# Optimization experiments

Measured on AMD Instinct MI355X. Metric: run time of the kernel, lower is better.

## Reference

```python
import jax, jax.numpy as jnp
import numpy as np

NUM_CLUSTERS = 64  # label vocabulary size (labels in [0, NUM_CLUSTERS))


def setup_inputs() -> dict:
    key = jax.random.key(0)
    kf, kl = jax.random.split(key)
    features = jax.random.normal(kf, (8192, 128), dtype=jnp.float32)
    labels = jax.random.randint(kl, (8192,), 0, NUM_CLUSTERS, dtype=jnp.int64)
    return {"features": features, "labels": labels}


def _pairwise_dist(x):
    # Euclidean cdist with a grad-safe sqrt (zero entries -> zero, no NaN grads).
    sq = jnp.sum(x * x, axis=-1)                      # [N]
    d2 = sq[:, None] + sq[None, :] - 2.0 * (x @ x.T)  # [N, N]
    d2 = jnp.maximum(d2, 0.0)
    pos = d2 > 0
    return jnp.sqrt(jnp.where(pos, d2, 1.0)) * pos.astype(x.dtype)


def reference(features, labels):
    N = features.shape[0]
    C = NUM_CLUSTERS
    dtype = features.dtype

    onehot = jax.nn.one_hot(labels, C, dtype=dtype)   # [N, C]
    counts = jnp.sum(onehot, axis=0)                  # [C]

    dists = _pairwise_dist(features)                  # [N, N]
    # Per-sample sum of distances to each cluster: segment-sum over columns.
    S = dists @ onehot                                # [N, C]

    own_count = counts[labels]                        # [N]
    idx = jnp.arange(N)
    # mean intra-cluster distance a_i (exclude self: divide by n-1)
    a = S[idx, labels] / jnp.maximum(own_count - 1.0, 1.0)

    # mean distance to every other cluster; mask own cluster and empty clusters
    mean_inter = S / jnp.maximum(counts, 1.0)[None, :]          # [N, C]
    invalid = (onehot > 0) | (counts[None, :] == 0)
    big = jnp.asarray(jnp.finfo(dtype).max, dtype)
    b = jnp.min(jnp.where(invalid, big, mean_inter), axis=1)    # [N]

    score = (b - a) / jnp.maximum(b, a)
    # singleton clusters get score 0 (matches torch branch num_elements <= 1)
    score = jnp.where(own_count > 1, score, jnp.zeros((), dtype))
    return jnp.mean(score)
```

## Files before the change

### kernel.cpp

```cpp
#include <hip/hip_runtime.h>
#include <hip/hip_fp16.h>
#include <float.h>

#define NC 64
#define FD 128
#define LSTR 136

typedef _Float16 f16x8 __attribute__((ext_vector_type(8)));
typedef float f32x4 __attribute__((ext_vector_type(4)));

__global__ void prep_kernel(const float* __restrict__ feat,
                            const int* __restrict__ labels,
                            float* __restrict__ sq,
                            unsigned short* __restrict__ Xh,
                            unsigned short* __restrict__ Mt,
                            float* __restrict__ S,
                            float* __restrict__ out, int out_size,
                            int* __restrict__ counts, int N) {
  __shared__ int hist[NC];
  int t = threadIdx.x;
  if (t < NC) hist[t] = 0;
  __syncthreads();
  int row = blockIdx.x * 32 + (t >> 3);
  int o = t & 7;
  if (row < N) {
    const float* rp = feat + (size_t)row * FD;
    float s = 0.f;
#pragma unroll
    for (int j = 0; j < 4; ++j) {
      int c4 = o + 8 * j;
      float4 v = *(const float4*)(rp + c4 * 4);
      ushort4 h;
      h.x = __half_as_ushort(__float2half(v.x));
      h.y = __half_as_ushort(__float2half(v.y));
      h.z = __half_as_ushort(__float2half(v.z));
      h.w = __half_as_ushort(__float2half(v.w));
      *(ushort4*)&Xh[(size_t)row * FD + c4 * 4] = h;
      s = fmaf(v.x, v.x, s); s = fmaf(v.y, v.y, s);
      s = fmaf(v.z, v.z, s); s = fmaf(v.w, v.w, s);
    }
    s += __shfl_xor(s, 1); s += __shfl_xor(s, 2); s += __shfl_xor(s, 4);
    if (o == 0) { sq[row] = s; atomicAdd(&hist[labels[row]], 1); }
  }
  if ((blockIdx.x + 1) * 32 <= N) {
    float4 z = {0.f, 0.f, 0.f, 0.f};
    size_t base = (size_t)blockIdx.x * 32 * NC + t * 8;
    *(float4*)&S[base] = z;
    *(float4*)&S[base + 4] = z;
  }
  if (blockIdx.x == 0 && t < out_size) out[t] = 0.f;
  {
    int chunksPerN = N >> 3;
    int total = NC * chunksPerN;
    for (int id = blockIdx.x * 256 + t; id < total; id += gridDim.x * 256) {
      int n = id / chunksPerN;
      int c0 = (id - n * chunksPerN) * 8;
      ushort4 lo, hi;
      lo.x = (labels[c0 + 0] == n) ? 0x3C00 : 0;
      lo.y = (labels[c0 + 1] == n) ? 0x3C00 : 0;
      lo.z = (labels[c0 + 2] == n) ? 0x3C00 : 0;
      lo.w = (labels[c0 + 3] == n) ? 0x3C00 : 0;
      hi.x = (labels[c0 + 4] == n) ? 0x3C00 : 0;
      hi.y = (labels[c0 + 5] == n) ? 0x3C00 : 0;
      hi.z = (labels[c0 + 6] == n) ? 0x3C00 : 0;
      hi.w = (labels[c0 + 7] == n) ? 0x3C00 : 0;
      *(ushort4*)&Mt[(size_t)n * N + c0] = lo;
      *(ushort4*)&Mt[(size_t)n * N + c0 + 4] = hi;
    }
  }
  __syncthreads();
  if (t < NC) atomicAdd(&counts[t], hist[t]);
}

__global__ __launch_bounds__(256, 2)
void mfma_tile_kernel(const unsigned short* __restrict__ Xh,
                      const float* __restrict__ sq,
                      const unsigned short* __restrict__ Mt,
                      float* __restrict__ S,
                      int N, int colsPerSplit) {
  __shared__ __align__(16) unsigned short Ah[128 * LSTR];
  __shared__ __align__(16) unsigned short Bh[128 * LSTR];

  const int t = threadIdx.x;
  const int R = blockIdx.x * 128;
  const int cBeg = blockIdx.y * colsPerSplit;
  const int wave = t >> 6, lane = t & 63;
  const int mm = lane & 15, quad = lane >> 4;
  const int wr = wave >> 1, wc = wave & 1;

#pragma unroll
  for (int it = 0; it < 8; ++it) {
    int c = t + it * 256;
    int r = c >> 4, k0 = (c & 15) * 8;
    *(uint4*)&Ah[r * LSTR + k0] = *(const uint4*)&Xh[(size_t)(R + r) * FD + k0];
  }
  float sqi_r[4];
#pragma unroll
  for (int ib = 0; ib < 4; ++ib)
    sqi_r[ib] = sq[R + wr * 64 + ib * 16 + mm];

  f32x4 sacc[2][4];
#pragma unroll
  for (int rt = 0; rt < 2; ++rt)
#pragma unroll
    for (int lt = 0; lt < 4; ++lt) sacc[rt][lt] = (f32x4)0.f;

  const int numTiles = colsPerSplit / 128;
  for (int ct = 0; ct < numTiles; ++ct) {
    const int C0 = cBeg + ct * 128;
    __syncthreads();
#pragma unroll
    for (int it = 0; it < 8; ++it) {
      int c = t + it * 256;
      int r = c >> 4, k0 = (c & 15) * 8;
      *(uint4*)&Bh[r * LSTR + k0] = *(const uint4*)&Xh[(size_t)(C0 + r) * FD + k0];
    }
    float sjr[4][4];
#pragma unroll
    for (int jb = 0; jb < 4; ++jb)
#pragma unroll
      for (int r = 0; r < 4; ++r)
        sjr[jb][r] = sq[C0 + wc * 64 + jb * 16 + quad * 4 + r];
    __syncthreads();

    f32x4 dacc[4][4];
#pragma unroll
    for (int ib = 0; ib < 4; ++ib)
#pragma unroll
      for (int jb = 0; jb < 4; ++jb) dacc[ib][jb] = (f32x4)0.f;

#pragma unroll
    for (int ks = 0; ks < 4; ++ks) {
      const int ko = ks * 32 + quad * 8;
      f16x8 af[4], bf[4];
#pragma unroll
      for (int ib = 0; ib < 4; ++ib)
        af[ib] = *(const f16x8*)&Ah[(wr * 64 + ib * 16 + mm) * LSTR + ko];
#pragma unroll
      for (int jb = 0; jb < 4; ++jb)
        bf[jb] = *(const f16x8*)&Bh[(wc * 64 + jb * 16 + mm) * LSTR + ko];
#pragma unroll
      for (int ib = 0; ib < 4; ++ib)
#pragma unroll
        for (int jb = 0; jb < 4; ++jb)
          dacc[ib][jb] = __builtin_amdgcn_mfma_f32_16x16x32_f16(bf[jb], af[ib], dacc[ib][jb], 0, 0, 0);
    }
    __syncthreads();

    const bool hasDiag = (R == C0);
#pragma unroll
    for (int ib = 0; ib < 4; ++ib) {
      const int rowLocal = wr * 64 + ib * 16 + mm;
      const float si = sqi_r[ib];
#pragma unroll
      for (int jb = 0; jb < 4; ++jb) {
        const int colBase = wc * 64 + jb * 16 + quad * 4;
        float d[4];
#pragma unroll
        for (int r = 0; r < 4; ++r) {
          float d2 = fmaf(-2.f, dacc[ib][jb][r], si + sjr[jb][r]);
          d[r] = __builtin_amdgcn_sqrtf(fmaxf(d2, 0.f));
        }
        if (hasDiag) {
#pragma unroll
          for (int r = 0; r < 4; ++r)
            if (rowLocal == colBase + r) d[r] = 0.f;
        }
        uint2 pk;
        pk.x = __builtin_bit_cast(unsigned, __builtin_amdgcn_cvt_pkrtz(d[0], d[1]));
        pk.y = __builtin_bit_cast(unsigned, __builtin_amdgcn_cvt_pkrtz(d[2], d[3]));
        *(uint2*)&Bh[rowLocal * LSTR + colBase] = pk;
      }
    }
    __syncthreads();

#pragma unroll
    for (int ks = 0; ks < 4; ++ks) {
      const int ko = ks * 32 + quad * 8;
      f16x8 da0 = *(const f16x8*)&Bh[(wave * 32 + mm) * LSTR + ko];
      f16x8 da1 = *(const f16x8*)&Bh[(wave * 32 + 16 + mm) * LSTR + ko];
#pragma unroll
      for (int lt = 0; lt < 4; ++lt) {
        f16x8 mb = *(const f16x8*)&Mt[(size_t)(lt * 16 + mm) * N + C0 + ks * 32 + quad * 8];
        sacc[0][lt] = __builtin_amdgcn_mfma_f32_16x16x32_f16(da0, mb, sacc[0][lt], 0, 0, 0);
        sacc[1][lt] = __builtin_amdgcn_mfma_f32_16x16x32_f16(da1, mb, sacc[1][lt], 0, 0, 0);
      }
    }
  }

#pragma unroll
  for (int rt = 0; rt < 2; ++rt)
#pragma unroll
    for (int lt = 0; lt < 4; ++lt)
#pragma unroll
      for (int r = 0; r < 4; ++r) {
        int row = wave * 32 + rt * 16 + quad * 4 + r;
        atomicAdd(&S[(size_t)(R + row) * NC + lt * 16 + mm], sacc[rt][lt][r]);
      }
}

__global__ void score_kernel(const float* __restrict__ S,
                             const int* __restrict__ labels,
                             const int* __restrict__ counts,
                             float* __restrict__ out, int N) {
  __shared__ float cnt_s[NC];
  __shared__ float inv_s[NC];
  __shared__ float red[128];
  int t = threadIdx.x;
  if (t < NC) {
    float c = (float)counts[t];
    cnt_s[t] = c;
    inv_s[t] = 1.f / fmaxf(c, 1.f);
  }
  __syncthreads();
  int i = blockIdx.x * 128 + t;
  float score = 0.f;
  if (i < N) {
    int li = labels[i];
    float own = cnt_s[li];
    const float4* Sv = (const float4*)(S + (size_t)i * NC);
    float a = S[(size_t)i * NC + li] / fmaxf(own - 1.f, 1.f);
    float b = FLT_MAX;
#pragma unroll
    for (int c4 = 0; c4 < NC / 4; ++c4) {
      float4 v = Sv[c4];
      int c = c4 * 4;
      float m0 = v.x * inv_s[c + 0];
      float m1 = v.y * inv_s[c + 1];
      float m2 = v.z * inv_s[c + 2];
      float m3 = v.w * inv_s[c + 3];
      b = fminf(b, (c + 0 == li || cnt_s[c + 0] == 0.f) ? FLT_MAX : m0);
      b = fminf(b, (c + 1 == li || cnt_s[c + 1] == 0.f) ? FLT_MAX : m1);
      b = fminf(b, (c + 2 == li || cnt_s[c + 2] == 0.f) ? FLT_MAX : m2);
      b = fminf(b, (c + 3 == li || cnt_s[c + 3] == 0.f) ? FLT_MAX : m3);
    }
    float mx = fmaxf(a, b);
    score = (own > 1.f) ? (b - a) / mx : 0.f;
  }
  red[t] = score;
  __syncthreads();
  for (int sft = 64; sft > 0; sft >>= 1) {
    if (t < sft) red[t] += red[t + sft];
    __syncthreads();
  }
  if (t == 0) atomicAdd(out, red[0] / (float)N);
}

extern "C" void kernel_launch(void* const* d_in, const int* in_sizes, int n_in,
                              void* d_out, int out_size, void* d_ws, size_t ws_size,
                              hipStream_t stream) {
  const float* feat = (const float*)d_in[0];
  const int* labels = (const int*)d_in[1];
  const int N = in_sizes[1];
  float* out = (float*)d_out;
  char* ws = (char*)d_ws;

  int*   counts = (int*)ws;
  float* sq     = (float*)(ws + 256);
  size_t o = 256 + (size_t)N * 4;
  o = (o + 255) & ~(size_t)255;
  unsigned short* Xh = (unsigned short*)(ws + o);
  unsigned short* Mt = (unsigned short*)(ws + o + (size_t)N * FD * 2);
  float* S = (float*)(ws + o + (size_t)N * FD * 2 + (size_t)NC * N * 2);

  (void)hipMemsetAsync(counts, 0, 256, stream);

  prep_kernel<<<(N + 31) / 32, 256, 0, stream>>>(feat, labels, sq, Xh, Mt, S,
                                                 out, out_size, counts, N);

  const int colSplit = 8;
  dim3 grid(N / 128, colSplit);
  mfma_tile_kernel<<<grid, 256, 0, stream>>>(Xh, sq, Mt, S, N, N / colSplit);

  score_kernel<<<(N + 127) / 128, 128, 0, stream>>>(S, labels, counts, out, N);
}
```

Baseline: 126.0 us.

## Double-buffer B tiles with async global-to-LDS loads and XOR swizzle

Replaces the padded shared-memory layout with an XOR-swizzled 128x128 layout and double-buffers the column tile. Global loads now go directly to LDS, so the next tile is fetched while the current one is being computed. The A-row fragments are kept in registers for the whole kernel instead of being re-read from LDS. This aims to hide global load latency and cut LDS traffic. In exchange it raises register pressure (16 f16x8 A fragments held live), and relying on the async load completing before the barrier is subtle.

New measurement: 137.4 us. 1.09x slower.

```diff
diff --git a/kernel.cpp b/kernel.cpp
--- a/kernel.cpp
+++ b/kernel.cpp
@@ -4,7 +4,6 @@
 
 #define NC 64
 #define FD 128
-#define LSTR 136
 
 typedef _Float16 f16x8 __attribute__((ext_vector_type(8)));
 typedef float f32x4 __attribute__((ext_vector_type(4)));
@@ -72,14 +71,23 @@
   if (t < NC) atomicAdd(&counts[t], hist[t]);
 }
 
+__device__ __forceinline__ int swz(int row, int chunk, int rem) {
+  return row * 256 + ((chunk ^ (row & 7)) << 4) + rem;
+}
+
+__device__ __forceinline__ void gload_lds16(const unsigned short* g, unsigned short* l) {
+  __builtin_amdgcn_global_load_lds(
+      (const __attribute__((address_space(1))) void*)g,
+      (__attribute__((address_space(3))) void*)l, 16, 0, 0);
+}
+
 __global__ __launch_bounds__(256, 2)
 void mfma_tile_kernel(const unsigned short* __restrict__ Xh,
                       const float* __restrict__ sq,
                       const unsigned short* __restrict__ Mt,
                       float* __restrict__ S,
                       int N, int colsPerSplit) {
-  __shared__ __align__(16) unsigned short Ah[128 * LSTR];
-  __shared__ __align__(16) unsigned short Bh[128 * LSTR];
+  __shared__ __align__(16) unsigned short Bh[2][128 * 128];
 
   const int t = threadIdx.x;
   const int R = blockIdx.x * 128;
@@ -87,13 +95,30 @@
   const int wave = t >> 6, lane = t & 63;
   const int mm = lane & 15, quad = lane >> 4;
   const int wr = wave >> 1, wc = wave & 1;
-
-#pragma unroll
-  for (int it = 0; it < 8; ++it) {
-    int c = t + it * 256;
-    int r = c >> 4, k0 = (c & 15) * 8;
-    *(uint4*)&Ah[r * LSTR + k0] = *(const uint4*)&Xh[(size_t)(R + r) * FD + k0];
-  }
+  const int numTiles = colsPerSplit / 128;
+
+#define STAGE(buf, C0base)                                                    \
+  {                                                                           \
+    const int rB_ = wave * 32;                                                \
+    _Pragma("unroll")                                                         \
+    for (int it_ = 0; it_ < 8; ++it_) {                                       \
+      const int rloc_ = rB_ + it_ * 4 + (lane >> 4);                          \
+      const int cch_ = lane & 15;                                             \
+      const unsigned short* g_ =                                              \
+          &Xh[(size_t)((C0base) + rloc_) * FD + ((cch_ ^ (rloc_ & 7)) << 3)]; \
+      unsigned short* l_ = &Bh[buf][(size_t)(rB_ + it_ * 4) * 128];           \
+      gload_lds16(g_, l_);                                                    \
+    }                                                                         \
+  }
+
+  f16x8 af[4][4];
+#pragma unroll
+  for (int ib = 0; ib < 4; ++ib)
+#pragma unroll
+    for (int ks = 0; ks < 4; ++ks)
+      af[ib][ks] = *(const f16x8*)&Xh[(size_t)(R + wr * 64 + ib * 16 + mm) * FD
+                                      + ks * 32 + quad * 8];
+
   float sqi_r[4];
 #pragma unroll
   for (int ib = 0; ib < 4; ++ib)
@@ -105,23 +130,20 @@
 #pragma unroll
     for (int lt = 0; lt < 4; ++lt) sacc[rt][lt] = (f32x4)0.f;
 
-  const int numTiles = colsPerSplit / 128;
+  STAGE(0, cBeg);
+  __syncthreads();
+
+  int cur = 0;
   for (int ct = 0; ct < numTiles; ++ct) {
     const int C0 = cBeg + ct * 128;
-    __syncthreads();
-#pragma unroll
-    for (int it = 0; it < 8; ++it) {
-      int c = t + it * 256;
-      int r = c >> 4, k0 = (c & 15) * 8;
-      *(uint4*)&Bh[r * LSTR + k0] = *(const uint4*)&Xh[(size_t)(C0 + r) * FD + k0];
-    }
+    if (ct + 1 < numTiles) STAGE(cur ^ 1, C0 + 128);
+
     float sjr[4][4];
 #pragma unroll
     for (int jb = 0; jb < 4; ++jb)
 #pragma unroll
       for (int r = 0; r < 4; ++r)
         sjr[jb][r] = sq[C0 + wc * 64 + jb * 16 + quad * 4 + r];
-    __syncthreads();
 
     f32x4 dacc[4][4];
 #pragma unroll
@@ -131,19 +153,18 @@
 
 #pragma unroll
     for (int ks = 0; ks < 4; ++ks) {
-      const int ko = ks * 32 + quad * 8;
-      f16x8 af[4], bf[4];
+      f16x8 bf[4];
+#pragma unroll
+      for (int jb = 0; jb < 4; ++jb) {
+        const int rowB = wc * 64 + jb * 16 + mm;
+        bf[jb] = *(const f16x8*)((const char*)&Bh[cur][0]
+                                 + swz(rowB, ks * 4 + quad, 0));
+      }
 #pragma unroll
       for (int ib = 0; ib < 4; ++ib)
-        af[ib] = *(const f16x8*)&Ah[(wr * 64 + ib * 16 + mm) * LSTR + ko];
-#pragma unroll
-      for (int jb = 0; jb < 4; ++jb)
-        bf[jb] = *(const f16x8*)&Bh[(wc * 64 + jb * 16 + mm) * LSTR + ko];
-#pragma unroll
-      for (int ib = 0; ib < 4; ++ib)
 #pragma unroll
         for (int jb = 0; jb < 4; ++jb)
-          dacc[ib][jb] = __builtin_amdgcn_mfma_f32_16x16x32_f16(bf[jb], af[ib], dacc[ib][jb], 0, 0, 0);
+          dacc[ib][jb] = __builtin_amdgcn_mfma_f32_16x16x32_f16(bf[jb], af[ib][ks], dacc[ib][jb], 0, 0, 0);
     }
     __syncthreads();
 
@@ -169,16 +190,17 @@
         uint2 pk;
         pk.x = __builtin_bit_cast(unsigned, __builtin_amdgcn_cvt_pkrtz(d[0], d[1]));
         pk.y = __builtin_bit_cast(unsigned, __builtin_amdgcn_cvt_pkrtz(d[2], d[3]));
-        *(uint2*)&Bh[rowLocal * LSTR + colBase] = pk;
+        const int chunk = wc * 8 + jb * 2 + (quad >> 1);
+        *(uint2*)((char*)&Bh[cur][0] + swz(rowLocal, chunk, (quad & 1) * 8)) = pk;
       }
     }
     __syncthreads();
 
 #pragma unroll
     for (int ks = 0; ks < 4; ++ks) {
-      const int ko = ks * 32 + quad * 8;
-      f16x8 da0 = *(const f16x8*)&Bh[(wave * 32 + mm) * LSTR + ko];
-      f16x8 da1 = *(const f16x8*)&Bh[(wave * 32 + 16 + mm) * LSTR + ko];
+      const int r0 = wave * 32 + mm;
+      f16x8 da0 = *(const f16x8*)((const char*)&Bh[cur][0] + swz(r0, ks * 4 + quad, 0));
+      f16x8 da1 = *(const f16x8*)((const char*)&Bh[cur][0] + swz(r0 + 16, ks * 4 + quad, 0));
 #pragma unroll
       for (int lt = 0; lt < 4; ++lt) {
         f16x8 mb = *(const f16x8*)&Mt[(size_t)(lt * 16 + mm) * N + C0 + ks * 32 + quad * 8];
@@ -186,6 +208,8 @@
         sacc[1][lt] = __builtin_amdgcn_mfma_f32_16x16x32_f16(da1, mb, sacc[1][lt], 0, 0, 0);
       }
     }
+    __syncthreads();
+    cur ^= 1;
   }
 
 #pragma unroll
@@ -197,6 +221,7 @@
         int row = wave * 32 + rt * 16 + quad * 4 + r;
         atomicAdd(&S[(size_t)(R + row) * NC + lt * 16 + mm], sacc[rt][lt][r]);
       }
+#undef STAGE
 }
 
 __global__ void score_kernel(const float* __restrict__ S,
```
